# Kernel tuning notes

Measured on AMD Instinct MI355X. Metric: run time of the kernel, lower is better.

The kernel has to match this reference:

```python
import jax, jax.numpy as jnp
import numpy as np

B = 256      # batch
D = 31       # per-mode feature dim (before bias-1 column)
FUSED = (D + 1) ** 3  # 32768
H1, H2, NCLS = 1024, 256, 4


def setup_inputs() -> dict:
    key = jax.random.key(0)
    ks = jax.random.split(key, 9)
    s = lambda fan_in: 1.0 / np.sqrt(fan_in)
    return {
        "x0": jax.random.normal(ks[0], (B, D), dtype=jnp.float32),
        "x1": jax.random.normal(ks[1], (B, D), dtype=jnp.float32),
        "x2": jax.random.normal(ks[2], (B, D), dtype=jnp.float32),
        "W1": jax.random.uniform(ks[3], (FUSED, H1), jnp.float32, -s(FUSED), s(FUSED)),
        "b1": jax.random.uniform(ks[4], (H1,), jnp.float32, -s(FUSED), s(FUSED)),
        "W2": jax.random.uniform(ks[5], (H1, H2), jnp.float32, -s(H1), s(H1)),
        "b2": jax.random.uniform(ks[6], (H2,), jnp.float32, -s(H1), s(H1)),
        "W3": jax.random.uniform(ks[7], (H2, NCLS), jnp.float32, -s(H2), s(H2)),
        "b3": jax.random.uniform(ks[8], (NCLS,), jnp.float32, -s(H2), s(H2)),
    }


def reference(x0, x1, x2, W1, b1, W2, b2, W3, b3):
    ones = jnp.ones((x0.shape[0], 1), dtype=x0.dtype)
    z0 = jnp.concatenate([x0, ones], axis=1)  # [B, D+1]
    z1 = jnp.concatenate([x1, ones], axis=1)
    z2 = jnp.concatenate([x2, ones], axis=1)
    # Batched triple outer product (vectorized over B, replacing the per-sample loop)
    fused = jnp.einsum("bi,bj,bk->bijk", z0, z1, z2).reshape(x0.shape[0], -1)  # [B, (D+1)^3]
    h = jax.nn.relu(fused @ W1 + b1)
    h = jax.nn.relu(h @ W2 + b2)
    return h @ W3 + b3  # [B, NCLS]
```

## Files before the change

kernel.cpp:

```cpp
#include <hip/hip_runtime.h>


typedef _Float16 half8 __attribute__((ext_vector_type(8)));
typedef _Float16 half4 __attribute__((ext_vector_type(4)));
typedef _Float16 half2 __attribute__((ext_vector_type(2)));
typedef float f32x4 __attribute__((ext_vector_type(4)));
typedef float f32x2 __attribute__((ext_vector_type(2)));

#define KSPLIT 32

__global__ __launch_bounds__(512, 4) void k1_gemm(
    const float* __restrict__ x0, const float* __restrict__ x1,
    const float* __restrict__ x2, const float* __restrict__ W1,
    _Float16* __restrict__ partial)
{
    __shared__ _Float16 z1L[256 * 36];
    __shared__ _Float16 tile[4][64 * 36];

    const int tid  = threadIdx.x;
    const int nt   = blockIdx.x & 15;
    const int ks   = blockIdx.x >> 4;
    const int lane = tid & 63;
    const int w    = tid >> 6;
    const int nl   = lane & 15;
    const int g    = lane >> 4;
    const int mh   = w >> 1;
    const int nw   = w & 1;
    const int n0   = nt * 64;

    for (int idx = tid; idx < 256 * 32; idx += 512) {
        int b = idx >> 5, j = idx & 31;
        z1L[b * 36 + j] = (_Float16)((j < 31) ? x1[b * 31 + j] : 1.0f);
    }

    half8 z2v[4];
#pragma unroll
    for (int ms = 0; ms < 4; ++ms) {
        int b = mh * 64 + ms * 16 + nl;
        float v0 = (ks < 31) ? x0[b * 31 + ks] : 1.0f;
#pragma unroll
        for (int e = 0; e < 8; ++e) {
            int kp = g * 8 + e;
            float v2 = (kp < 31) ? x2[b * 31 + kp] : 1.0f;
            z2v[ms][e] = (_Float16)(v0 * v2);
        }
    }

    const int sn = tid & 63;
    const float* gp = W1 + ((size_t)ks * 1024 + 4 * w) * 1024 + n0 + sn;
    const int woff = sn * 36 + 4 * w;

    const int roff0 = (nw * 32 + nl) * 36 + g * 8;
    const int roff1 = (nw * 32 + 16 + nl) * 36 + g * 8;

    float rq[4][4];
#pragma unroll
    for (int s = 0; s < 3; ++s) {
#pragma unroll
        for (int q = 0; q < 4; ++q) rq[s][q] = gp[q * 1024];
        gp += 32768;
    }
    {
        half2 h01, h23;
        h01[0] = (_Float16)rq[0][0]; h01[1] = (_Float16)rq[0][1];
        h23[0] = (_Float16)rq[0][2]; h23[1] = (_Float16)rq[0][3];
        *(half2*)&tile[0][woff]     = h01;
        *(half2*)&tile[0][woff + 2] = h23;
    }
    asm volatile("s_waitcnt lgkmcnt(0)\n\ts_barrier" ::: "memory");

    f32x4 acc[4][2] = {};
    half4 z1q[4];

#define STEP(TT, ISSUE, WRITE, T0)                                             \
    {                                                                          \
        if (ISSUE) {                                                           \
            _Pragma("unroll")                                                  \
            for (int q = 0; q < 4; ++q) rq[((TT) + 3) & 3][q] = gp[q * 1024];  \
            gp += 32768;                                                       \
        }                                                                      \
        if ((TT) == 0) {                                                       \
            _Pragma("unroll")                                                  \
            for (int ms = 0; ms < 4; ++ms)                                     \
                z1q[ms] = *(const half4*)&z1L[(mh * 64 + ms * 16 + nl) * 36 + (T0)]; \
        }                                                                      \
        const _Float16* tb = &tile[(TT) & 3][0];                               \
        half4 lo0 = *(const half4*)&tb[roff0];                                 \
        half4 hi0 = *(const half4*)&tb[roff0 + 4];                             \
        half4 lo1 = *(const half4*)&tb[roff1];                                 \
        half4 hi1 = *(const half4*)&tb[roff1 + 4];                             \
        half8 bh0 = __builtin_shufflevector(lo0, hi0, 0,1,2,3,4,5,6,7);        \
        half8 bh1 = __builtin_shufflevector(lo1, hi1, 0,1,2,3,4,5,6,7);        \
        _Pragma("unroll")                                                      \
        for (int ms = 0; ms < 4; ++ms) {                                       \
            half8 a = z2v[ms] * z1q[ms][TT];                                   \
            acc[ms][0] = __builtin_amdgcn_mfma_f32_16x16x32_f16(a, bh0, acc[ms][0], 0, 0, 0); \
            acc[ms][1] = __builtin_amdgcn_mfma_f32_16x16x32_f16(a, bh1, acc[ms][1], 0, 0, 0); \
        }                                                                      \
        if (WRITE) {                                                           \
            const float* s = rq[((TT) + 1) & 3];                               \
            half2 h01, h23;                                                    \
            h01[0] = (_Float16)s[0]; h01[1] = (_Float16)s[1];                  \
            h23[0] = (_Float16)s[2]; h23[1] = (_Float16)s[3];                  \
            _Float16* tw = &tile[((TT) + 1) & 3][0];                           \
            *(half2*)&tw[woff]     = h01;                                      \
            *(half2*)&tw[woff + 2] = h23;                                      \
        }                                                                      \
        asm volatile("s_waitcnt lgkmcnt(0)\n\ts_barrier" ::: "memory");        \
    }

    for (int grp = 0; grp < 7; ++grp) {
        const int t0 = grp * 4;
        STEP(0, 1, 1, t0)
        STEP(1, 1, 1, t0)
        STEP(2, 1, 1, t0)
        STEP(3, 1, 1, t0)
    }
    STEP(0, 1, 1, 28)
    STEP(1, 0, 1, 28)
    STEP(2, 0, 1, 28)
    STEP(3, 0, 0, 28)
#undef STEP

    _Float16* pbase = partial + ((size_t)ks << 18);
#pragma unroll
    for (int ms = 0; ms < 4; ++ms)
#pragma unroll
        for (int ns = 0; ns < 2; ++ns) {
            int h = n0 + nw * 32 + ns * 16 + nl;
            int b0 = mh * 64 + ms * 16 + g * 4;
#pragma unroll
            for (int r = 0; r < 4; ++r)
                pbase[(b0 + r) * 1024 + h] = (_Float16)acc[ms][ns][r];
        }
}

__global__ __launch_bounds__(256) void k2_reduce(
    const _Float16* __restrict__ partial, const float* __restrict__ b1,
    float* __restrict__ h1)
{
    int e2 = blockIdx.x * 256 + threadIdx.x;
    const half2* pv = (const half2*)partial;
    float s0 = 0.f, s1 = 0.f;
#pragma unroll
    for (int sp = 0; sp < KSPLIT; ++sp) {
        half2 v = pv[(size_t)sp * 131072 + e2];
        s0 += (float)v[0]; s1 += (float)v[1];
    }
    int h = (e2 * 2) & 1023;
    f32x2 o;
    o[0] = fmaxf(s0 + b1[h], 0.f);
    o[1] = fmaxf(s1 + b1[h + 1], 0.f);
    *(f32x2*)&h1[e2 * 2] = o;
}

__global__ __launch_bounds__(256) void k3_layer2(
    const float* __restrict__ h1, const float* __restrict__ W2,
    float* __restrict__ p2)
{
    __shared__ float h1t[32 * 129];
    __shared__ float w2t[128 * 65];
    const int tid = threadIdx.x;
    const int m0 = blockIdx.x * 32, n0 = blockIdx.y * 64, k0 = blockIdx.z * 128;

    for (int idx = tid; idx < 32 * 128; idx += 256) {
        int m = idx >> 7, kk = idx & 127;
        h1t[m * 129 + kk] = h1[(m0 + m) * 1024 + k0 + kk];
    }
    for (int idx = tid; idx < 128 * 64; idx += 256) {
        int kk = idx >> 6, n = idx & 63;
        w2t[kk * 65 + n] = W2[(k0 + kk) * 256 + n0 + n];
    }
    __syncthreads();

    const int tn = tid & 63, tm = tid >> 6;
    float acc[8] = {};
    for (int kk = 0; kk < 128; ++kk) {
        float wv = w2t[kk * 65 + tn];
#pragma unroll
        for (int r = 0; r < 8; ++r)
            acc[r] += h1t[(tm * 8 + r) * 129 + kk] * wv;
    }
#pragma unroll
    for (int r = 0; r < 8; ++r)
        p2[blockIdx.z * 65536 + (m0 + tm * 8 + r) * 256 + n0 + tn] = acc[r];
}

__global__ __launch_bounds__(256) void k4_final(
    const float* __restrict__ p2, const float* __restrict__ b2,
    const float* __restrict__ W3, const float* __restrict__ b3,
    float* __restrict__ out)
{
    __shared__ float pL[256 * 5];
    const int b = blockIdx.x, n = threadIdx.x;
    float s = 0.f;
#pragma unroll
    for (int sp = 0; sp < 8; ++sp) s += p2[sp * 65536 + b * 256 + n];
    float h2 = fmaxf(s + b2[n], 0.f);
#pragma unroll
    for (int ccls = 0; ccls < 4; ++ccls) pL[n * 5 + ccls] = h2 * W3[n * 4 + ccls];
    __syncthreads();

    const int lane = n & 63, w = n >> 6;
    float v = pL[lane * 5 + w] + pL[(lane + 64) * 5 + w] +
              pL[(lane + 128) * 5 + w] + pL[(lane + 192) * 5 + w];
#pragma unroll
    for (int off = 32; off > 0; off >>= 1) v += __shfl_down(v, off);
    if (lane == 0) out[b * 4 + w] = v + b3[w];
}

extern "C" void kernel_launch(void* const* d_in, const int* in_sizes, int n_in,
                              void* d_out, int out_size, void* d_ws, size_t ws_size,
                              hipStream_t stream)
{
    (void)in_sizes; (void)n_in; (void)out_size; (void)ws_size;
    const float* x0 = (const float*)d_in[0];
    const float* x1 = (const float*)d_in[1];
    const float* x2 = (const float*)d_in[2];
    const float* W1 = (const float*)d_in[3];
    const float* b1 = (const float*)d_in[4];
    const float* W2 = (const float*)d_in[5];
    const float* b2 = (const float*)d_in[6];
    const float* W3 = (const float*)d_in[7];
    const float* b3 = (const float*)d_in[8];
    float* out = (float*)d_out;

    _Float16* partial = (_Float16*)d_ws;
    float* h1 = (float*)((char*)d_ws + (size_t)KSPLIT * 262144 * 2);
    float* p2 = h1 + 262144;

    k1_gemm  <<<dim3(512),     dim3(512), 0, stream>>>(x0, x1, x2, W1, partial);
    k2_reduce<<<dim3(512),     dim3(256), 0, stream>>>(partial, b1, h1);
    k3_layer2<<<dim3(8, 4, 8), dim3(256), 0, stream>>>(h1, W2, p2);
    k4_final <<<dim3(256),     dim3(256), 0, stream>>>(p2, b2, W3, b3, out);
}
```

Before: 54.56 us.

## Reduce layer-1 K-split to 8 with narrower N tiles and per-warp batch rows

Layer-1 GEMM now splits K eight ways instead of thirty-two. Each block covers four x0 indices (4096 K rows) and 32 output columns, with every wave owning 32 batch rows. This shrinks the fp16 partial buffer the reduce kernel must read and write. In exchange the grid drops to 256 blocks with fewer independent waves, and each block runs a much longer serial loop with a barrier per step. k2_reduce reads KSPLIT, so it automatically sums fewer partials.

```diff
diff --git a/kernel.cpp b/kernel.cpp
--- a/kernel.cpp
+++ b/kernel.cpp
@@ -7,128 +7,141 @@
 typedef float f32x4 __attribute__((ext_vector_type(4)));
 typedef float f32x2 __attribute__((ext_vector_type(2)));
 
-#define KSPLIT 32
-
-__global__ __launch_bounds__(512, 4) void k1_gemm(
+#define KSPLIT 8
+
+__global__ __launch_bounds__(512, 2) void k1_gemm(
     const float* __restrict__ x0, const float* __restrict__ x1,
     const float* __restrict__ x2, const float* __restrict__ W1,
     _Float16* __restrict__ partial)
 {
     __shared__ _Float16 z1L[256 * 36];
-    __shared__ _Float16 tile[4][64 * 36];
+    __shared__ _Float16 z0L[4 * 256];
+    __shared__ _Float16 tile[4][32 * 36];
 
     const int tid  = threadIdx.x;
-    const int nt   = blockIdx.x & 15;
-    const int ks   = blockIdx.x >> 4;
+    const int nt   = blockIdx.x & 31;
+    const int ks   = blockIdx.x >> 5;
     const int lane = tid & 63;
     const int w    = tid >> 6;
     const int nl   = lane & 15;
     const int g    = lane >> 4;
-    const int mh   = w >> 1;
-    const int nw   = w & 1;
-    const int n0   = nt * 64;
+    const int kbase = ks * 4096;
+    const int n0    = nt * 32;
 
     for (int idx = tid; idx < 256 * 32; idx += 512) {
         int b = idx >> 5, j = idx & 31;
         z1L[b * 36 + j] = (_Float16)((j < 31) ? x1[b * 31 + j] : 1.0f);
     }
-
-    half8 z2v[4];
-#pragma unroll
-    for (int ms = 0; ms < 4; ++ms) {
-        int b = mh * 64 + ms * 16 + nl;
-        float v0 = (ks < 31) ? x0[b * 31 + ks] : 1.0f;
+    for (int idx = tid; idx < 4 * 256; idx += 512) {
+        int ii = idx >> 8, b = idx & 255;
+        int i = ks * 4 + ii;
+        z0L[ii * 256 + b] = (_Float16)((i < 31) ? x0[b * 31 + i] : 1.0f);
+    }
+
+    half8 z2v[2];
+#pragma unroll
+    for (int ms = 0; ms < 2; ++ms) {
+        int b = w * 32 + ms * 16 + nl;
 #pragma unroll
         for (int e = 0; e < 8; ++e) {
             int kp = g * 8 + e;
-            float v2 = (kp < 31) ? x2[b * 31 + kp] : 1.0f;
-            z2v[ms][e] = (_Float16)(v0 * v2);
+            z2v[ms][e] = (_Float16)((kp < 31) ? x2[b * 31 + kp] : 1.0f);
         }
     }
 
-    const int sn = tid & 63;
-    const float* gp = W1 + ((size_t)ks * 1024 + 4 * w) * 1024 + n0 + sn;
-    const int woff = sn * 36 + 4 * w;
-
-    const int roff0 = (nw * 32 + nl) * 36 + g * 8;
-    const int roff1 = (nw * 32 + 16 + nl) * 36 + g * 8;
-
-    float rq[4][4];
+    const int sn = tid & 31;
+    const int sk = tid >> 5;
+    const float* gp = W1 + ((size_t)kbase + 2 * sk) * 1024 + n0 + sn;
+    const int woff = sn * 36 + 2 * sk;
+
+    const int roff0 = nl * 36 + g * 8;
+    const int roff1 = (16 + nl) * 36 + g * 8;
+
+    __syncthreads();
+
+    float rq[4][2];
 #pragma unroll
     for (int s = 0; s < 3; ++s) {
-#pragma unroll
-        for (int q = 0; q < 4; ++q) rq[s][q] = gp[q * 1024];
+        rq[s][0] = gp[0];
+        rq[s][1] = gp[1024];
         gp += 32768;
     }
     {
-        half2 h01, h23;
-        h01[0] = (_Float16)rq[0][0]; h01[1] = (_Float16)rq[0][1];
-        h23[0] = (_Float16)rq[0][2]; h23[1] = (_Float16)rq[0][3];
-        *(half2*)&tile[0][woff]     = h01;
-        *(half2*)&tile[0][woff + 2] = h23;
+        half2 hv; hv[0] = (_Float16)rq[0][0]; hv[1] = (_Float16)rq[0][1];
+        *(half2*)&tile[0][woff] = hv;
     }
     asm volatile("s_waitcnt lgkmcnt(0)\n\ts_barrier" ::: "memory");
 
-    f32x4 acc[4][2] = {};
-    half4 z1q[4];
-
-#define STEP(TT, ISSUE, WRITE, T0)                                             \
-    {                                                                          \
-        if (ISSUE) {                                                           \
-            _Pragma("unroll")                                                  \
-            for (int q = 0; q < 4; ++q) rq[((TT) + 3) & 3][q] = gp[q * 1024];  \
-            gp += 32768;                                                       \
-        }                                                                      \
-        if ((TT) == 0) {                                                       \
-            _Pragma("unroll")                                                  \
-            for (int ms = 0; ms < 4; ++ms)                                     \
-                z1q[ms] = *(const half4*)&z1L[(mh * 64 + ms * 16 + nl) * 36 + (T0)]; \
-        }                                                                      \
-        const _Float16* tb = &tile[(TT) & 3][0];                               \
-        half4 lo0 = *(const half4*)&tb[roff0];                                 \
-        half4 hi0 = *(const half4*)&tb[roff0 + 4];                             \
-        half4 lo1 = *(const half4*)&tb[roff1];                                 \
-        half4 hi1 = *(const half4*)&tb[roff1 + 4];                             \
-        half8 bh0 = __builtin_shufflevector(lo0, hi0, 0,1,2,3,4,5,6,7);        \
-        half8 bh1 = __builtin_shufflevector(lo1, hi1, 0,1,2,3,4,5,6,7);        \
-        _Pragma("unroll")                                                      \
-        for (int ms = 0; ms < 4; ++ms) {                                       \
-            half8 a = z2v[ms] * z1q[ms][TT];                                   \
+    f32x4 acc[2][2] = {};
+    half4 z01q[2];
+    _Float16 z0s[2];
+
+#define STEP(TT, ISSUE, WRITE, T0)                                            \
+    {                                                                         \
+        if (ISSUE) {                                                          \
+            rq[((TT) + 3) & 3][0] = gp[0];                                    \
+            rq[((TT) + 3) & 3][1] = gp[1024];                                 \
+            gp += 32768;                                                      \
+        }                                                                     \
+        if ((TT) == 0) {                                                      \
+            _Pragma("unroll")                                                 \
+            for (int ms = 0; ms < 2; ++ms) {                                  \
+                half4 zq = *(const half4*)&z1L[(w * 32 + ms * 16 + nl) * 36   \
+                                               + ((T0) & 31)];                \
+                z01q[ms] = zq * z0s[ms];                                      \
+            }                                                                 \
+        }                                                                     \
+        const _Float16* tb = &tile[(TT) & 3][0];                              \
+        half4 lo0 = *(const half4*)&tb[roff0];                                \
+        half4 hi0 = *(const half4*)&tb[roff0 + 4];                            \
+        half4 lo1 = *(const half4*)&tb[roff1];                                \
+        half4 hi1 = *(const half4*)&tb[roff1 + 4];                            \
+        half8 bh0 = __builtin_shufflevector(lo0, hi0, 0,1,2,3,4,5,6,7);       \
+        half8 bh1 = __builtin_shufflevector(lo1, hi1, 0,1,2,3,4,5,6,7);       \
+        _Pragma("unroll")                                                     \
+        for (int ms = 0; ms < 2; ++ms) {                                      \
+            half8 a = z2v[ms] * z01q[ms][TT];                                 \
             acc[ms][0] = __builtin_amdgcn_mfma_f32_16x16x32_f16(a, bh0, acc[ms][0], 0, 0, 0); \
             acc[ms][1] = __builtin_amdgcn_mfma_f32_16x16x32_f16(a, bh1, acc[ms][1], 0, 0, 0); \
-        }                                                                      \
-        if (WRITE) {                                                           \
-            const float* s = rq[((TT) + 1) & 3];                               \
-            half2 h01, h23;                                                    \
-            h01[0] = (_Float16)s[0]; h01[1] = (_Float16)s[1];                  \
-            h23[0] = (_Float16)s[2]; h23[1] = (_Float16)s[3];                  \
-            _Float16* tw = &tile[((TT) + 1) & 3][0];                           \
-            *(half2*)&tw[woff]     = h01;                                      \
-            *(half2*)&tw[woff + 2] = h23;                                      \
-        }                                                                      \
-        asm volatile("s_waitcnt lgkmcnt(0)\n\ts_barrier" ::: "memory");        \
-    }
-
-    for (int grp = 0; grp < 7; ++grp) {
-        const int t0 = grp * 4;
+        }                                                                     \
+        if (WRITE) {                                                          \
+            half2 hv;                                                         \
+            hv[0] = (_Float16)rq[((TT) + 1) & 3][0];                          \
+            hv[1] = (_Float16)rq[((TT) + 1) & 3][1];                          \
+            *(half2*)&tile[((TT) + 1) & 3][woff] = hv;                        \
+        }                                                                     \
+        asm volatile("s_waitcnt lgkmcnt(0)\n\ts_barrier" ::: "memory");       \
+    }
+
+    for (int ii = 0; ii < 4; ++ii) {
+#pragma unroll
+        for (int ms = 0; ms < 2; ++ms)
+            z0s[ms] = z0L[ii * 256 + w * 32 + ms * 16 + nl];
+        const int qmax = (ii == 3) ? 7 : 8;
+        for (int q = 0; q < qmax; ++q) {
+            const int t0 = ii * 32 + q * 4;
+            STEP(0, 1, 1, t0)
+            STEP(1, 1, 1, t0)
+            STEP(2, 1, 1, t0)
+            STEP(3, 1, 1, t0)
+        }
+    }
+    {
+        const int t0 = 124;
         STEP(0, 1, 1, t0)
-        STEP(1, 1, 1, t0)
-        STEP(2, 1, 1, t0)
-        STEP(3, 1, 1, t0)
-    }
-    STEP(0, 1, 1, 28)
-    STEP(1, 0, 1, 28)
-    STEP(2, 0, 1, 28)
-    STEP(3, 0, 0, 28)
+        STEP(1, 0, 1, t0)
+        STEP(2, 0, 1, t0)
+        STEP(3, 0, 0, t0)
+    }
 #undef STEP
 
     _Float16* pbase = partial + ((size_t)ks << 18);
 #pragma unroll
-    for (int ms = 0; ms < 4; ++ms)
+    for (int ms = 0; ms < 2; ++ms)
 #pragma unroll
         for (int ns = 0; ns < 2; ++ns) {
-            int h = n0 + nw * 32 + ns * 16 + nl;
-            int b0 = mh * 64 + ms * 16 + g * 4;
+            int h = n0 + ns * 16 + nl;
+            int b0 = w * 32 + ms * 16 + g * 4;
 #pragma unroll
             for (int r = 0; r < 4; ++r)
                 pbase[(b0 + r) * 1024 + h] = (_Float16)acc[ms][ns][r];
@@ -229,7 +242,7 @@
     float* h1 = (float*)((char*)d_ws + (size_t)KSPLIT * 262144 * 2);
     float* p2 = h1 + 262144;
 
-    k1_gemm  <<<dim3(512),     dim3(512), 0, stream>>>(x0, x1, x2, W1, partial);
+    k1_gemm  <<<dim3(256),     dim3(512), 0, stream>>>(x0, x1, x2, W1, partial);
     k2_reduce<<<dim3(512),     dim3(256), 0, stream>>>(partial, b1, h1);
     k3_layer2<<<dim3(8, 4, 8), dim3(256), 0, stream>>>(h1, W2, p2);
     k4_final <<<dim3(256),     dim3(256), 0, stream>>>(p2, b2, W3, b3, out);
```

After: 56.32 us. 3.2% more time.
